# Kernel tuning notes

Hardware: AMD Instinct MI355X
Metric: run time of the kernel (lower is better)

## Reference

```python
import jax, jax.numpy as jnp
import numpy as np

HEADS = 20
HEAD_DIM = 64
NUM_IP = 20          # num_content_tokens (4) + num_style_tokens (16)
FU_SCALE = 0.5
STYLE_SCALE = 1.0
SCALE = 1.0 / np.sqrt(HEAD_DIM).astype(np.float32)


def setup_inputs() -> dict:
    key = jax.random.key(0)
    ks = jax.random.split(key, 9)
    B, S, H, C = 4, 4096, 1280, 2048
    T = 77 + NUM_IP  # text tokens + ip tokens
    w = 0.02
    return {
        "hidden_states": jax.random.normal(ks[0], (B, S, H), jnp.float32),
        "encoder_hidden_states": jax.random.normal(ks[1], (B, T, C), jnp.float32),
        "Wq": jax.random.normal(ks[2], (H, H), jnp.float32) * w,
        "Wk": jax.random.normal(ks[3], (H, C), jnp.float32) * w,
        "Wv": jax.random.normal(ks[4], (H, C), jnp.float32) * w,
        "Wk_ip": jax.random.normal(ks[5], (H, C), jnp.float32) * w,
        "Wv_ip": jax.random.normal(ks[6], (H, C), jnp.float32) * w,
        "Wo": jax.random.normal(ks[7], (H, H), jnp.float32) * w,
        "bo": jnp.zeros((H,), jnp.float32),
    }


def _to_heads(x):
    # [B, T, H] -> [B, heads, T, head_dim]
    B, T, _ = x.shape
    return x.reshape(B, T, HEADS, HEAD_DIM).transpose(0, 2, 1, 3)


def _blend(p):
    # cross-batch prob fusion: rows 1<-0, 3<-2 (CFG pairs)
    p = p.at[1].set(FU_SCALE * p[1] + (1.0 - FU_SCALE) * p[0])
    p = p.at[3].set(FU_SCALE * p[3] + (1.0 - FU_SCALE) * p[2])
    return p


def reference(hidden_states, encoder_hidden_states, Wq, Wk, Wv, Wk_ip, Wv_ip, Wo, bo):
    B, S, H = hidden_states.shape
    text = encoder_hidden_states[:, :-NUM_IP, :]   # [B, 77, C]
    ip = encoder_hidden_states[:, -NUM_IP:, :]     # [B, 20, C]

    q = _to_heads(hidden_states @ Wq.T)            # [B, h, S, d]
    k = _to_heads(text @ Wk.T)                     # [B, h, 77, d]
    v = _to_heads(text @ Wv.T)

    # fuAttn branch: explicit probs, blended across batch, then PV matmul
    probs = jax.nn.softmax(jnp.einsum('bhqd,bhkd->bhqk', q, k) * SCALE, axis=-1)
    probs = _blend(probs)
    raw = jnp.einsum('bhqk,bhkd->bhqd', probs, v)
    raw = raw.transpose(0, 2, 1, 3).reshape(B, S, H)

    # IP-adapter style cross-attention (fuIPAttn branch)
    ip_k = _to_heads(ip @ Wk_ip.T)                 # [B, h, 20, d]
    ip_v = _to_heads(ip @ Wv_ip.T)
    ip_probs = jax.nn.softmax(jnp.einsum('bhqd,bhkd->bhqk', q, ip_k) * SCALE, axis=-1)
    ip_probs = _blend(ip_probs)
    ip_hs = jnp.einsum('bhqk,bhkd->bhqd', ip_probs, ip_v)
    ip_hs = ip_hs.transpose(0, 2, 1, 3).reshape(B, S, H)

    hs = raw + STYLE_SCALE * ip_hs
    # batch rows 0 and 2 keep raw (text-only) attention output
    hs = hs.at[0].set(raw[0]).at[2].set(raw[2])

    # to_out[0] linear (bias) + to_out[1] dropout (identity at inference)
    return hs @ Wo.T + bo
```

## Files before the change

### kernel.cpp

```cpp
#include <hip/hip_runtime.h>
#include <cstdint>

typedef float floatx4 __attribute__((ext_vector_type(4)));
typedef __bf16 bf16x8 __attribute__((ext_vector_type(8)));

typedef const __attribute__((address_space(1))) void* gas_cvp;
typedef __attribute__((address_space(3))) void* las_vp;

__device__ __forceinline__ float bflo(unsigned int u) {
    return __builtin_bit_cast(float, u << 16);
}
__device__ __forceinline__ float bfhi(unsigned int u) {
    return __builtin_bit_cast(float, u & 0xffff0000u);
}
__device__ __forceinline__ unsigned short f2bf(float f) {
    unsigned int u = __builtin_bit_cast(unsigned int, f);
    u += 0x7fffu + ((u >> 16) & 1u);
    return (unsigned short)(u >> 16);
}
__device__ __forceinline__ bf16x8 ld8(const unsigned short* p) {
    return __builtin_bit_cast(bf16x8, *(const uint4*)p);
}
__device__ __forceinline__ floatx4 mfma32(bf16x8 a, bf16x8 b, floatx4 c) {
    return __builtin_amdgcn_mfma_f32_16x16x32_bf16(a, b, c, 0, 0, 0);
}
__device__ __forceinline__ void load_lds16(const void* g, void* l) {
    __builtin_amdgcn_global_load_lds(
        (gas_cvp)(unsigned long long)g,
        (las_vp)(unsigned int)(unsigned long long)l,
        16, 0, 0);
}

__global__ void cvt_f32_bf16(const float* __restrict__ in,
                             unsigned short* __restrict__ out, int n4) {
    int i = blockIdx.x * 256 + threadIdx.x;
    if (i < n4) {
        float4 v = ((const float4*)in)[i];
        ushort4 o;
        o.x = f2bf(v.x); o.y = f2bf(v.y); o.z = f2bf(v.z); o.w = f2bf(v.w);
        ((ushort4*)out)[i] = o;
    }
}

struct CvtJob { const float* src; unsigned short* dst; int n4; };
struct CvtJobs { CvtJob j[7]; };

__global__ void cvt_multi(CvtJobs jobs) {
    CvtJob jb = jobs.j[blockIdx.y];
    int i = blockIdx.x * 256 + threadIdx.x;
    if (i < jb.n4) {
        float4 v = ((const float4*)jb.src)[i];
        ushort4 o;
        o.x = f2bf(v.x); o.y = f2bf(v.y); o.z = f2bf(v.z); o.w = f2bf(v.w);
        ((ushort4*)jb.dst)[i] = o;
    }
}

struct GJob {
    const unsigned short* A;
    const unsigned short* B;
    void* C;
    int M, K;
    int rpb, bstride, roff;
    int bstart;
};
struct GArgs { GJob j[5]; };

#define GBAR() do { __builtin_amdgcn_s_barrier(); __builtin_amdgcn_sched_barrier(0); } while (0)

template <bool F32OUT>
__global__ __launch_bounds__(512, 2) void gemm256(GArgs args,
                                                  const float* __restrict__ bias) {
    const int tid = threadIdx.x;
    int jid = 0;
#pragma unroll
    for (int t = 1; t < 5; ++t)
        if ((int)blockIdx.x >= args.j[t].bstart) jid = t;
    const GJob jb = args.j[jid];
    const int K = jb.K;
    int b = (int)blockIdx.x - jb.bstart;
    {
        const int mt = (jb.M + 255) >> 8;
        const int nblk = mt * 5;
        if ((nblk & 7) == 0) b = (b & 7) * (nblk >> 3) + (b >> 3);
    }
    const int by = b / 5, bx = b - by * 5;

    __shared__ unsigned short ldsA[32768];
    __shared__ unsigned short ldsB[32768];

    const int srow   = ((tid >> 7) << 4) + ((tid >> 2) & 15);
    const int schunk = ((tid & 3) << 4) ^ (((tid >> 2) & 6) << 3);
    const int scol   = (((tid >> 6) & 1) << 5) + (schunk >> 1);

    const int Mloc = jb.M, rpbL = jb.rpb, bstrL = jb.bstride, roffL = jb.roff;
    auto maprow = [&](int r) -> size_t {
        r = (r < Mloc) ? r : (Mloc - 1);
        int blk = r / rpbL;
        return (size_t)(blk * bstrL + roffL + (r - blk * rpbL));
    };

    const unsigned short* pA[2][2];
    const unsigned short* pB[2][2];
    unsigned short* dA[2][2];
    unsigned short* dB[2][2];
#pragma unroll
    for (int h = 0; h < 2; ++h)
#pragma unroll
        for (int j = 0; j < 2; ++j) {
            const int r = h * 128 + j * 64 + srow;
            pA[h][j] = jb.A + maprow(by * 256 + r) * K + scol;
            pB[h][j] = jb.B + (size_t)(bx * 256 + r) * K + scol;
            dA[h][j] = &ldsA[h * 8192 + j * 4096 + tid * 8];
            dB[h][j] = &ldsB[h * 8192 + j * 4096 + tid * 8];
        }

    const int lane = tid & 63, fr = lane & 15, g = lane >> 4;
    const int w = tid >> 6, wr = w & 1, wc = w >> 1;
    const int rb   = fr * 32 + ((g * 8) ^ ((fr & 6) << 2));
    const int aoff = wr * 8192 + rb;
    const int boff = (wc >> 1) * 8192 + (wc & 1) * 4096 + rb;

    floatx4 acc[8][4] = {};
    bf16x8 af[4][2], bn0[2][2], bn1[2][2];

    const int KT = K >> 6;

    load_lds16(pA[0][0], dA[0][0]); load_lds16(pA[0][1], dA[0][1]);
    load_lds16(pA[1][0], dA[1][0]); load_lds16(pA[1][1], dA[1][1]);
    load_lds16(pB[0][0], dB[0][0]); load_lds16(pB[0][1], dB[0][1]);
    load_lds16(pB[1][0], dB[1][0]); load_lds16(pB[1][1], dB[1][1]);
    load_lds16(pB[0][0] + 64, dB[0][0] + 16384);
    load_lds16(pB[0][1] + 64, dB[0][1] + 16384);
    load_lds16(pA[0][0] + 64, dA[0][0] + 16384);
    load_lds16(pA[0][1] + 64, dA[0][1] + 16384);
    asm volatile("s_waitcnt vmcnt(4)" ::: "memory");
    GBAR();

    for (int u = 0; u < KT; ++u) {
        const int pb = (u & 1) << 14;
        const int qb = pb ^ 16384;
        const int k1 = (u + 1 < KT) ? (u + 1) : (KT - 1);
        const int k2 = (u + 2 < KT) ? (u + 2) : (KT - 1);

#pragma unroll
        for (int mi = 0; mi < 4; ++mi)
#pragma unroll
            for (int kk = 0; kk < 2; ++kk)
                af[mi][kk] = *(const bf16x8*)&ldsA[pb + aoff + (mi * 2 + kk) * 512];
#pragma unroll
        for (int nf = 0; nf < 2; ++nf)
#pragma unroll
            for (int kk = 0; kk < 2; ++kk)
                bn0[nf][kk] = *(const bf16x8*)&ldsB[pb + boff + (nf * 2 + kk) * 512];
        load_lds16(pA[1][0] + (size_t)k1 * 64, dA[1][0] + qb);
        load_lds16(pA[1][1] + (size_t)k1 * 64, dA[1][1] + qb);
        GBAR();
        __builtin_amdgcn_s_setprio(1);
#pragma unroll
        for (int kk = 0; kk < 2; ++kk)
#pragma unroll
            for (int mi = 0; mi < 4; ++mi)
#pragma unroll
                for (int nf = 0; nf < 2; ++nf)
                    acc[mi][nf] = mfma32(af[mi][kk], bn0[nf][kk], acc[mi][nf]);
        __builtin_amdgcn_s_setprio(0);
        GBAR();

#pragma unroll
        for (int nf = 0; nf < 2; ++nf)
#pragma unroll
            for (int kk = 0; kk < 2; ++kk)
                bn1[nf][kk] = *(const bf16x8*)&ldsB[pb + boff + ((nf + 2) * 2 + kk) * 512];
        load_lds16(pB[1][0] + (size_t)k1 * 64, dB[1][0] + qb);
        load_lds16(pB[1][1] + (size_t)k1 * 64, dB[1][1] + qb);
        GBAR();
        __builtin_amdgcn_s_setprio(1);
#pragma unroll
        for (int kk = 0; kk < 2; ++kk)
#pragma unroll
            for (int mi = 0; mi < 4; ++mi)
#pragma unroll
                for (int nf = 0; nf < 2; ++nf)
                    acc[mi][nf + 2] = mfma32(af[mi][kk], bn1[nf][kk], acc[mi][nf + 2]);
        __builtin_amdgcn_s_setprio(0);
        GBAR();

#pragma unroll
        for (int mi = 0; mi < 4; ++mi)
#pragma unroll
            for (int kk = 0; kk < 2; ++kk)
                af[mi][kk] = *(const bf16x8*)&ldsA[pb + aoff + ((mi + 4) * 2 + kk) * 512];
        load_lds16(pB[0][0] + (size_t)k2 * 64, dB[0][0] + pb);
        load_lds16(pB[0][1] + (size_t)k2 * 64, dB[0][1] + pb);
        GBAR();
        __builtin_amdgcn_s_setprio(1);
#pragma unroll
        for (int kk = 0; kk < 2; ++kk)
#pragma unroll
            for (int mi = 0; mi < 4; ++mi)
#pragma unroll
                for (int nf = 0; nf < 2; ++nf)
                    acc[mi + 4][nf + 2] = mfma32(af[mi][kk], bn1[nf][kk], acc[mi + 4][nf + 2]);
        __builtin_amdgcn_s_setprio(0);
        GBAR();

        load_lds16(pA[0][0] + (size_t)k2 * 64, dA[0][0] + pb);
        load_lds16(pA[0][1] + (size_t)k2 * 64, dA[0][1] + pb);
        GBAR();
        __builtin_amdgcn_s_setprio(1);
#pragma unroll
        for (int kk = 0; kk < 2; ++kk)
#pragma unroll
            for (int mi = 0; mi < 4; ++mi)
#pragma unroll
                for (int nf = 0; nf < 2; ++nf)
                    acc[mi + 4][nf] = mfma32(af[mi][kk], bn0[nf][kk], acc[mi + 4][nf]);
        __builtin_amdgcn_s_setprio(0);
        asm volatile("s_waitcnt vmcnt(4)" ::: "memory");
        GBAR();
    }
    asm volatile("s_waitcnt vmcnt(0)" ::: "memory");

    const int colBase = bx * 256 + wc * 64;
    const int rowBase = by * 256 + wr * 128;
    float bv[4] = {};
    if (F32OUT) {
#pragma unroll
        for (int nf = 0; nf < 4; ++nf) bv[nf] = bias[colBase + nf * 16 + fr];
    }
#pragma unroll
    for (int mi = 0; mi < 8; ++mi) {
#pragma unroll
        for (int nf = 0; nf < 4; ++nf) {
            const int col  = colBase + nf * 16 + fr;
            const int row0 = rowBase + mi * 16 + g * 4;
#pragma unroll
            for (int r = 0; r < 4; ++r) {
                const int row = row0 + r;
                if (row < Mloc) {
                    float v = acc[mi][nf][r];
                    if (F32OUT)
                        ((float*)jb.C)[(size_t)row * 1280 + col] = v + bv[nf];
                    else
                        ((unsigned short*)jb.C)[(size_t)row * 1280 + col] = f2bf(v);
                }
            }
        }
    }
}

#define NT 77
#define NI 20
#define VSTR 104
#define ISTR 40

__global__ __launch_bounds__(256, 2) void attn_mfma(
    const unsigned short* __restrict__ q,
    const unsigned short* __restrict__ kt,
    const unsigned short* __restrict__ vt,
    const unsigned short* __restrict__ kip,
    const unsigned short* __restrict__ vip,
    unsigned short* __restrict__ outp)
{
    const int tid = threadIdx.x;
    const int qt = blockIdx.x;
    const int h  = blockIdx.y;
    const int pz = blockIdx.z;
    const int b0 = 2 * pz;
    const int lane  = tid & 63;
    const int w     = tid >> 6;
    const int bi    = w >> 1;
    const int strip = (w & 1) * 16;
    const int fr = lane & 15;
    const int g  = lane >> 4;

    __shared__ unsigned short sVt[2][64][VSTR];
    __shared__ unsigned short sVipt[2][64][ISTR];
    __shared__ unsigned short sP[2][32][VSTR];

    for (int i = tid; i < 2 * 64 * (VSTR - NT); i += 256) {
        int b = i / (64 * (VSTR - NT)); int rem = i % (64 * (VSTR - NT));
        sVt[b][rem / (VSTR - NT)][NT + rem % (VSTR - NT)] = 0;
    }
    for (int i = tid; i < 2 * 64 * (ISTR - NI); i += 256) {
        int b = i / (64 * (ISTR - NI)); int rem = i % (64 * (ISTR - NI));
        sVipt[b][rem / (ISTR - NI)][NI + rem % (ISTR - NI)] = 0;
    }
    for (int i = tid; i < 2 * 32 * (VSTR - 80); i += 256) {
        int b = i / (32 * (VSTR - 80)); int rem = i % (32 * (VSTR - 80));
        sP[b][rem / (VSTR - 80)][80 + rem % (VSTR - 80)] = 0;
    }

    for (int c = tid; c < 2 * 8 * NT; c += 256) {
        int b = c / (8 * NT); int rem = c % (8 * NT);
        int dc = rem / NT; int key = rem % NT;
        uint4 v = *(const uint4*)&vt[((size_t)((b0 + b) * NT + key)) * 1280 + h * 64 + dc * 8];
        unsigned int uu[4] = {v.x, v.y, v.z, v.w};
#pragma unroll
        for (int j = 0; j < 4; j++) {
            sVt[b][dc * 8 + 2 * j][key]     = (unsigned short)(uu[j] & 0xffffu);
            sVt[b][dc * 8 + 2 * j + 1][key] = (unsigned short)(uu[j] >> 16);
        }
    }
    for (int c = tid; c < 2 * 8 * NI; c += 256) {
        int b = c / (8 * NI); int rem = c % (8 * NI);
        int dc = rem / NI; int key = rem % NI;
        uint4 v = *(const uint4*)&vip[((size_t)((b0 + b) * NI + key)) * 1280 + h * 64 + dc * 8];
        unsigned int uu[4] = {v.x, v.y, v.z, v.w};
#pragma unroll
        for (int j = 0; j < 4; j++) {
            sVipt[b][dc * 8 + 2 * j][key]     = (unsigned short)(uu[j] & 0xffffu);
            sVipt[b][dc * 8 + 2 * j + 1][key] = (unsigned short)(uu[j] >> 16);
        }
    }

    const size_t qbase = ((size_t)((b0 + bi) * 4096 + qt * 32 + strip + fr)) * 1280 + h * 64;
    bf16x8 aq0 = ld8(&q[qbase + g * 8]);
    bf16x8 aq1 = ld8(&q[qbase + 32 + g * 8]);

    floatx4 sc[5] = {};
#pragma unroll
    for (int t = 0; t < 5; t++) {
        int key = t * 16 + fr; key = (key < NT) ? key : (NT - 1);
        const size_t kb = ((size_t)((b0 + bi) * NT + key)) * 1280 + h * 64;
        sc[t] = mfma32(aq0, ld8(&kt[kb + g * 8]), sc[t]);
        sc[t] = mfma32(aq1, ld8(&kt[kb + 32 + g * 8]), sc[t]);
    }

#pragma unroll
    for (int r = 0; r < 4; r++) {
        float m = -1e30f;
#pragma unroll
        for (int t = 0; t < 5; t++) {
            float v = sc[t][r] * 0.125f;
            if (t == 4 && fr >= 13) v = -1e30f;
            sc[t][r] = v;
            m = fmaxf(m, v);
        }
        m = fmaxf(m, __shfl_xor(m, 1));
        m = fmaxf(m, __shfl_xor(m, 2));
        m = fmaxf(m, __shfl_xor(m, 4));
        m = fmaxf(m, __shfl_xor(m, 8));
        float sum = 0.f;
#pragma unroll
        for (int t = 0; t < 5; t++) {
            float e = __expf(sc[t][r] - m);
            sc[t][r] = e;
            sum += e;
        }
        sum += __shfl_xor(sum, 1);
        sum += __shfl_xor(sum, 2);
        sum += __shfl_xor(sum, 4);
        sum += __shfl_xor(sum, 8);
        float inv = 1.f / sum;
#pragma unroll
        for (int t = 0; t < 5; t++)
            sP[bi][strip + g * 4 + r][t * 16 + fr] = f2bf(sc[t][r] * inv);
    }
    __syncthreads();

    {
        unsigned int* p0 = (unsigned int*)&sP[0][0][0];
        unsigned int* p1 = (unsigned int*)&sP[1][0][0];
        for (int i = tid; i < 32 * VSTR / 2; i += 256) {
            unsigned int a = p0[i], b = p1[i];
            unsigned short r0 = f2bf(0.5f * (bflo(a) + bflo(b)));
            unsigned short r1 = f2bf(0.5f * (bfhi(a) + bfhi(b)));
            p1[i] = (unsigned int)r0 | ((unsigned int)r1 << 16);
        }
    }
    __syncthreads();

    floatx4 accO[4] = {};
    {
        const unsigned short* prow = &sP[bi][strip + fr][0];
        bf16x8 pa0 = ld8(prow + g * 8);
        bf16x8 pa1 = ld8(prow + 32 + g * 8);
        bf16x8 pa2 = ld8(prow + 64 + g * 8);
#pragma unroll
        for (int dt = 0; dt < 4; dt++) {
            const unsigned short* vrow = &sVt[bi][dt * 16 + fr][0];
            accO[dt] = mfma32(pa0, ld8(vrow + g * 8), accO[dt]);
            accO[dt] = mfma32(pa1, ld8(vrow + 32 + g * 8), accO[dt]);
            accO[dt] = mfma32(pa2, ld8(vrow + 64 + g * 8), accO[dt]);
        }
    }

    floatx4 si[2] = {};
#pragma unroll
    for (int t = 0; t < 2; t++) {
        int key = t * 16 + fr; key = (key < NI) ? key : (NI - 1);
        const size_t kb = ((size_t)((b0 + bi) * NI + key)) * 1280 + h * 64;
        si[t] = mfma32(aq0, ld8(&kip[kb + g * 8]), si[t]);
        si[t] = mfma32(aq1, ld8(&kip[kb + 32 + g * 8]), si[t]);
    }
#pragma unroll
    for (int r = 0; r < 4; r++) {
        float v0 = si[0][r] * 0.125f;
        float v1 = (fr >= 4) ? -1e30f : si[1][r] * 0.125f;
        float m = fmaxf(v0, v1);
        m = fmaxf(m, __shfl_xor(m, 1));
        m = fmaxf(m, __shfl_xor(m, 2));
        m = fmaxf(m, __shfl_xor(m, 4));
        m = fmaxf(m, __shfl_xor(m, 8));
        float e0 = __expf(v0 - m), e1 = __expf(v1 - m);
        float s = e0 + e1;
        s += __shfl_xor(s, 1);
        s += __shfl_xor(s, 2);
        s += __shfl_xor(s, 4);
        s += __shfl_xor(s, 8);
        float inv = 1.f / s;
        si[0][r] = e0 * inv;
        si[1][r] = e1 * inv;
    }
    __syncthreads();

#pragma unroll
    for (int r = 0; r < 4; r++) {
        sP[bi][strip + g * 4 + r][fr]      = f2bf(si[0][r]);
        sP[bi][strip + g * 4 + r][16 + fr] = f2bf(si[1][r]);
    }
    __syncthreads();

    for (int i = tid; i < 32 * 16; i += 256) {
        int r = i >> 4, kk = i & 15;
        unsigned int* p0 = (unsigned int*)&sP[0][r][0];
        unsigned int* p1 = (unsigned int*)&sP[1][r][0];
        unsigned int a = p0[kk], b = p1[kk];
        unsigned short r0 = f2bf(0.5f * (bflo(a) + bflo(b)));
        unsigned short r1 = f2bf(0.5f * (bfhi(a) + bfhi(b)));
        p1[kk] = (unsigned int)r0 | ((unsigned int)r1 << 16);
    }
    __syncthreads();

    if (bi == 1) {
        const unsigned short* prow = &sP[1][strip + fr][0];
        bf16x8 pip = ld8(prow + g * 8);
#pragma unroll
        for (int dt = 0; dt < 4; dt++)
            accO[dt] = mfma32(pip, ld8(&sVipt[1][dt * 16 + fr][g * 8]), accO[dt]);
    }

    const size_t orow0 = (size_t)((b0 + bi) * 4096 + qt * 32 + strip);
#pragma unroll
    for (int dt = 0; dt < 4; dt++) {
        int col = h * 64 + dt * 16 + fr;
#pragma unroll
        for (int r = 0; r < 4; r++)
            outp[(orow0 + g * 4 + r) * 1280 + col] = f2bf(accO[dt][r]);
    }
}

extern "C" void kernel_launch(void* const* d_in, const int* in_sizes, int n_in,
                              void* d_out, int out_size, void* d_ws, size_t ws_size,
                              hipStream_t stream) {
    const float* hs   = (const float*)d_in[0];
    const float* ehs  = (const float*)d_in[1];
    const float* Wq   = (const float*)d_in[2];
    const float* Wk   = (const float*)d_in[3];
    const float* Wv   = (const float*)d_in[4];
    const float* Wkip = (const float*)d_in[5];
    const float* Wvip = (const float*)d_in[6];
    const float* Wo   = (const float*)d_in[7];
    const float* bo   = (const float*)d_in[8];

    char* w = (char*)d_ws;
    size_t off = 0;
    auto alloc = [&](size_t bytes) {
        char* pp = w + off;
        off += (bytes + 255) & ~(size_t)255;
        return pp;
    };
    unsigned short* hs_bf   = (unsigned short*)alloc(16384ull * 1280 * 2);
    unsigned short* q_bf    = (unsigned short*)alloc(16384ull * 1280 * 2);
    unsigned short* at_bf   = (unsigned short*)alloc(16384ull * 1280 * 2);
    unsigned short* ehs_bf  = (unsigned short*)alloc(4ull * 97 * 2048 * 2);
    unsigned short* Wq_bf   = (unsigned short*)alloc(1280ull * 1280 * 2);
    unsigned short* Wk_bf   = (unsigned short*)alloc(1280ull * 2048 * 2);
    unsigned short* Wv_bf   = (unsigned short*)alloc(1280ull * 2048 * 2);
    unsigned short* Wkip_bf = (unsigned short*)alloc(1280ull * 2048 * 2);
    unsigned short* Wvip_bf = (unsigned short*)alloc(1280ull * 2048 * 2);
    unsigned short* Wo_bf   = (unsigned short*)alloc(1280ull * 1280 * 2);
    unsigned short* kt  = (unsigned short*)alloc(308ull * 1280 * 2);
    unsigned short* vt  = (unsigned short*)alloc(308ull * 1280 * 2);
    unsigned short* kip = (unsigned short*)alloc(80ull * 1280 * 2);
    unsigned short* vip = (unsigned short*)alloc(80ull * 1280 * 2);

    cvt_f32_bf16<<<dim3(20480, 1, 1), 256, 0, stream>>>(hs, hs_bf, 16384 * 1280 / 4);

    CvtJobs cj{};
    cj.j[0] = CvtJob{ehs,  ehs_bf,  (int)(4ull * 97 * 2048 / 4)};
    cj.j[1] = CvtJob{Wq,   Wq_bf,   1280 * 1280 / 4};
    cj.j[2] = CvtJob{Wk,   Wk_bf,   1280 * 2048 / 4};
    cj.j[3] = CvtJob{Wv,   Wv_bf,   1280 * 2048 / 4};
    cj.j[4] = CvtJob{Wkip, Wkip_bf, 1280 * 2048 / 4};
    cj.j[5] = CvtJob{Wvip, Wvip_bf, 1280 * 2048 / 4};
    cj.j[6] = CvtJob{Wo,   Wo_bf,   1280 * 1280 / 4};
    cvt_multi<<<dim3(2560, 7, 1), 256, 0, stream>>>(cj);

    GArgs g1{};
    g1.j[0] = GJob{ehs_bf, Wk_bf,   (void*)kt,    308, 2048,    77, 97,  0,  0};
    g1.j[1] = GJob{ehs_bf, Wv_bf,   (void*)vt,    308, 2048,    77, 97,  0, 10};
    g1.j[2] = GJob{ehs_bf, Wkip_bf, (void*)kip,    80, 2048,    20, 97, 77, 20};
    g1.j[3] = GJob{ehs_bf, Wvip_bf, (void*)vip,    80, 2048,    20, 97, 77, 25};
    g1.j[4] = GJob{hs_bf,  Wq_bf,   (void*)q_bf, 16384, 1280, 16384,  0,  0, 30};
    gemm256<false><<<dim3(350, 1, 1), 512, 0, stream>>>(g1, nullptr);

    attn_mfma<<<dim3(128, 20, 2), 256, 0, stream>>>(q_bf, kt, vt, kip, vip, at_bf);

    GArgs g2{};
    g2.j[0] = GJob{at_bf, Wo_bf, d_out, 16384, 1280, 16384, 0, 0, 0};
    for (int t = 1; t < 5; ++t) g2.j[t].bstart = 0x7fffffff;
    gemm256<true><<<dim3(320, 1, 1), 512, 0, stream>>>(g2, bo);
}
```

Measured before the change: 442.8 us.

## Produce transposed padded V projections in GEMM to drop LDS transpose in attention

A new conversion kernel writes zero-padded text (96 rows per batch) and IP (32 rows per batch) token buffers. The V and IP-V projections are now computed as W·Xᵀ, so the GEMM writes them already transposed. The attention kernel then reads V straight from global memory instead of building transposed copies in LDS. This removes the per-block scatter transpose and most of the shared memory, so the attention kernel now asks for 4 blocks per CU instead of 2. The cost is uncached, strided global loads of V inside the PV MFMA loop and a little extra GEMM work on the padded rows.

```diff
diff --git a/kernel.cpp b/kernel.cpp
--- a/kernel.cpp
+++ b/kernel.cpp
@@ -43,7 +43,7 @@
 }
 
 struct CvtJob { const float* src; unsigned short* dst; int n4; };
-struct CvtJobs { CvtJob j[7]; };
+struct CvtJobs { CvtJob j[6]; };
 
 __global__ void cvt_multi(CvtJobs jobs) {
     CvtJob jb = jobs.j[blockIdx.y];
@@ -56,12 +56,42 @@
     }
 }
 
+__global__ void cvt_ehs(const float* __restrict__ ehs,
+                        unsigned short* __restrict__ text,
+                        unsigned short* __restrict__ ip) {
+    int i = blockIdx.x * 256 + threadIdx.x;
+    if (i < 384 * 512) {
+        int r = i >> 9, c = i & 511;
+        int b = r / 96, t = r - b * 96;
+        ushort4 o = {0, 0, 0, 0};
+        if (t < 77) {
+            float4 v = *(const float4*)&ehs[((size_t)(b * 97 + t)) * 2048 + c * 4];
+            o.x = f2bf(v.x); o.y = f2bf(v.y); o.z = f2bf(v.z); o.w = f2bf(v.w);
+        }
+        ((ushort4*)text)[i] = o;
+    } else {
+        int i2 = i - 384 * 512;
+        if (i2 < 128 * 512) {
+            int r = i2 >> 9, c = i2 & 511;
+            int b = r >> 5, t = r & 31;
+            ushort4 o = {0, 0, 0, 0};
+            if (t < 20) {
+                float4 v = *(const float4*)&ehs[((size_t)(b * 97 + 77 + t)) * 2048 + c * 4];
+                o.x = f2bf(v.x); o.y = f2bf(v.y); o.z = f2bf(v.z); o.w = f2bf(v.w);
+            }
+            ((ushort4*)ip)[i2] = o;
+        }
+    }
+}
+
 struct GJob {
     const unsigned short* A;
     const unsigned short* B;
     void* C;
     int M, K;
-    int rpb, bstride, roff;
+    int Bn;
+    int nt;
+    int ldc;
     int bstart;
 };
 struct GArgs { GJob j[5]; };
@@ -81,10 +111,10 @@
     int b = (int)blockIdx.x - jb.bstart;
     {
         const int mt = (jb.M + 255) >> 8;
-        const int nblk = mt * 5;
+        const int nblk = mt * jb.nt;
         if ((nblk & 7) == 0) b = (b & 7) * (nblk >> 3) + (b >> 3);
     }
-    const int by = b / 5, bx = b - by * 5;
+    const int by = b / jb.nt, bx = b - by * jb.nt;
 
     __shared__ unsigned short ldsA[32768];
     __shared__ unsigned short ldsB[32768];
@@ -93,12 +123,7 @@
     const int schunk = ((tid & 3) << 4) ^ (((tid >> 2) & 6) << 3);
     const int scol   = (((tid >> 6) & 1) << 5) + (schunk >> 1);
 
-    const int Mloc = jb.M, rpbL = jb.rpb, bstrL = jb.bstride, roffL = jb.roff;
-    auto maprow = [&](int r) -> size_t {
-        r = (r < Mloc) ? r : (Mloc - 1);
-        int blk = r / rpbL;
-        return (size_t)(blk * bstrL + roffL + (r - blk * rpbL));
-    };
+    const int Mloc = jb.M, BnL = jb.Bn;
 
     const unsigned short* pA[2][2];
     const unsigned short* pB[2][2];
@@ -109,8 +134,10 @@
 #pragma unroll
         for (int j = 0; j < 2; ++j) {
             const int r = h * 128 + j * 64 + srow;
-            pA[h][j] = jb.A + maprow(by * 256 + r) * K + scol;
-            pB[h][j] = jb.B + (size_t)(bx * 256 + r) * K + scol;
+            int ra = by * 256 + r;  ra = (ra < Mloc) ? ra : (Mloc - 1);
+            int rb2 = bx * 256 + r; rb2 = (rb2 < BnL) ? rb2 : (BnL - 1);
+            pA[h][j] = jb.A + (size_t)ra * K + scol;
+            pB[h][j] = jb.B + (size_t)rb2 * K + scol;
             dA[h][j] = &ldsA[h * 8192 + j * 4096 + tid * 8];
             dB[h][j] = &ldsB[h * 8192 + j * 4096 + tid * 8];
         }
@@ -224,6 +251,7 @@
 
     const int colBase = bx * 256 + wc * 64;
     const int rowBase = by * 256 + wr * 128;
+    const int ldc = jb.ldc;
     float bv[4] = {};
     if (F32OUT) {
 #pragma unroll
@@ -241,9 +269,9 @@
                 if (row < Mloc) {
                     float v = acc[mi][nf][r];
                     if (F32OUT)
-                        ((float*)jb.C)[(size_t)row * 1280 + col] = v + bv[nf];
+                        ((float*)jb.C)[(size_t)row * ldc + col] = v + bv[nf];
                     else
-                        ((unsigned short*)jb.C)[(size_t)row * 1280 + col] = f2bf(v);
+                        ((unsigned short*)jb.C)[(size_t)row * ldc + col] = f2bf(v);
                 }
             }
         }
@@ -252,15 +280,13 @@
 
 #define NT 77
 #define NI 20
-#define VSTR 104
-#define ISTR 40
-
-__global__ __launch_bounds__(256, 2) void attn_mfma(
+
+__global__ __launch_bounds__(256, 4) void attn_mfma(
     const unsigned short* __restrict__ q,
     const unsigned short* __restrict__ kt,
-    const unsigned short* __restrict__ vt,
+    const unsigned short* __restrict__ vtT,
     const unsigned short* __restrict__ kip,
-    const unsigned short* __restrict__ vip,
+    const unsigned short* __restrict__ ipT,
     unsigned short* __restrict__ outp)
 {
     const int tid = threadIdx.x;
@@ -275,44 +301,11 @@
     const int fr = lane & 15;
     const int g  = lane >> 4;
 
-    __shared__ unsigned short sVt[2][64][VSTR];
-    __shared__ unsigned short sVipt[2][64][ISTR];
-    __shared__ unsigned short sP[2][32][VSTR];
-
-    for (int i = tid; i < 2 * 64 * (VSTR - NT); i += 256) {
-        int b = i / (64 * (VSTR - NT)); int rem = i % (64 * (VSTR - NT));
-        sVt[b][rem / (VSTR - NT)][NT + rem % (VSTR - NT)] = 0;
-    }
-    for (int i = tid; i < 2 * 64 * (ISTR - NI); i += 256) {
-        int b = i / (64 * (ISTR - NI)); int rem = i % (64 * (ISTR - NI));
-        sVipt[b][rem / (ISTR - NI)][NI + rem % (ISTR - NI)] = 0;
-    }
-    for (int i = tid; i < 2 * 32 * (VSTR - 80); i += 256) {
-        int b = i / (32 * (VSTR - 80)); int rem = i % (32 * (VSTR - 80));
-        sP[b][rem / (VSTR - 80)][80 + rem % (VSTR - 80)] = 0;
-    }
-
-    for (int c = tid; c < 2 * 8 * NT; c += 256) {
-        int b = c / (8 * NT); int rem = c % (8 * NT);
-        int dc = rem / NT; int key = rem % NT;
-        uint4 v = *(const uint4*)&vt[((size_t)((b0 + b) * NT + key)) * 1280 + h * 64 + dc * 8];
-        unsigned int uu[4] = {v.x, v.y, v.z, v.w};
-#pragma unroll
-        for (int j = 0; j < 4; j++) {
-            sVt[b][dc * 8 + 2 * j][key]     = (unsigned short)(uu[j] & 0xffffu);
-            sVt[b][dc * 8 + 2 * j + 1][key] = (unsigned short)(uu[j] >> 16);
-        }
-    }
-    for (int c = tid; c < 2 * 8 * NI; c += 256) {
-        int b = c / (8 * NI); int rem = c % (8 * NI);
-        int dc = rem / NI; int key = rem % NI;
-        uint4 v = *(const uint4*)&vip[((size_t)((b0 + b) * NI + key)) * 1280 + h * 64 + dc * 8];
-        unsigned int uu[4] = {v.x, v.y, v.z, v.w};
-#pragma unroll
-        for (int j = 0; j < 4; j++) {
-            sVipt[b][dc * 8 + 2 * j][key]     = (unsigned short)(uu[j] & 0xffffu);
-            sVipt[b][dc * 8 + 2 * j + 1][key] = (unsigned short)(uu[j] >> 16);
-        }
+    __shared__ unsigned short sP[2][32][104];
+
+    for (int i = tid; i < 2 * 32 * 24; i += 256) {
+        int b = i / (32 * 24); int rem = i % (32 * 24);
+        sP[b][rem / 24][80 + rem % 24] = 0;
     }
 
     const size_t qbase = ((size_t)((b0 + bi) * 4096 + qt * 32 + strip + fr)) * 1280 + h * 64;
@@ -322,8 +315,8 @@
     floatx4 sc[5] = {};
 #pragma unroll
     for (int t = 0; t < 5; t++) {
-        int key = t * 16 + fr; key = (key < NT) ? key : (NT - 1);
-        const size_t kb = ((size_t)((b0 + bi) * NT + key)) * 1280 + h * 64;
+        int key = t * 16 + fr;
+        const size_t kb = ((size_t)((b0 + bi) * 96 + key)) * 1280 + h * 64;
         sc[t] = mfma32(aq0, ld8(&kt[kb + g * 8]), sc[t]);
         sc[t] = mfma32(aq1, ld8(&kt[kb + 32 + g * 8]), sc[t]);
     }
@@ -363,7 +356,7 @@
     {
         unsigned int* p0 = (unsigned int*)&sP[0][0][0];
         unsigned int* p1 = (unsigned int*)&sP[1][0][0];
-        for (int i = tid; i < 32 * VSTR / 2; i += 256) {
+        for (int i = tid; i < 32 * 104 / 2; i += 256) {
             unsigned int a = p0[i], b = p1[i];
             unsigned short r0 = f2bf(0.5f * (bflo(a) + bflo(b)));
             unsigned short r1 = f2bf(0.5f * (bfhi(a) + bfhi(b)));
@@ -378,9 +371,10 @@
         bf16x8 pa0 = ld8(prow + g * 8);
         bf16x8 pa1 = ld8(prow + 32 + g * 8);
         bf16x8 pa2 = ld8(prow + 64 + g * 8);
+        const int vcol = (b0 + bi) * 96;
 #pragma unroll
         for (int dt = 0; dt < 4; dt++) {
-            const unsigned short* vrow = &sVt[bi][dt * 16 + fr][0];
+            const unsigned short* vrow = &vtT[(size_t)(h * 64 + dt * 16 + fr) * 512 + vcol];
             accO[dt] = mfma32(pa0, ld8(vrow + g * 8), accO[dt]);
             accO[dt] = mfma32(pa1, ld8(vrow + 32 + g * 8), accO[dt]);
             accO[dt] = mfma32(pa2, ld8(vrow + 64 + g * 8), accO[dt]);
@@ -390,8 +384,8 @@
     floatx4 si[2] = {};
 #pragma unroll
     for (int t = 0; t < 2; t++) {
-        int key = t * 16 + fr; key = (key < NI) ? key : (NI - 1);
-        const size_t kb = ((size_t)((b0 + bi) * NI + key)) * 1280 + h * 64;
+        int key = t * 16 + fr;
+        const size_t kb = ((size_t)((b0 + bi) * 32 + key)) * 1280 + h * 64;
         si[t] = mfma32(aq0, ld8(&kip[kb + g * 8]), si[t]);
         si[t] = mfma32(aq1, ld8(&kip[kb + 32 + g * 8]), si[t]);
     }
@@ -437,9 +431,12 @@
     if (bi == 1) {
         const unsigned short* prow = &sP[1][strip + fr][0];
         bf16x8 pip = ld8(prow + g * 8);
+        const int icol = (b0 + 1) * 32;
 #pragma unroll
         for (int dt = 0; dt < 4; dt++)
-            accO[dt] = mfma32(pip, ld8(&sVipt[1][dt * 16 + fr][g * 8]), accO[dt]);
+            accO[dt] = mfma32(pip,
+                              ld8(&ipT[(size_t)(h * 64 + dt * 16 + fr) * 256 + icol + g * 8]),
+                              accO[dt]);
     }
 
     const size_t orow0 = (size_t)((b0 + bi) * 4096 + qt * 32 + strip);
@@ -475,42 +472,44 @@
     unsigned short* hs_bf   = (unsigned short*)alloc(16384ull * 1280 * 2);
     unsigned short* q_bf    = (unsigned short*)alloc(16384ull * 1280 * 2);
     unsigned short* at_bf   = (unsigned short*)alloc(16384ull * 1280 * 2);
-    unsigned short* ehs_bf  = (unsigned short*)alloc(4ull * 97 * 2048 * 2);
+    unsigned short* text_pad= (unsigned short*)alloc(384ull * 2048 * 2);
+    unsigned short* ip_pad  = (unsigned short*)alloc(128ull * 2048 * 2);
     unsigned short* Wq_bf   = (unsigned short*)alloc(1280ull * 1280 * 2);
     unsigned short* Wk_bf   = (unsigned short*)alloc(1280ull * 2048 * 2);
     unsigned short* Wv_bf   = (unsigned short*)alloc(1280ull * 2048 * 2);
     unsigned short* Wkip_bf = (unsigned short*)alloc(1280ull * 2048 * 2);
     unsigned short* Wvip_bf = (unsigned short*)alloc(1280ull * 2048 * 2);
     unsigned short* Wo_bf   = (unsigned short*)alloc(1280ull * 1280 * 2);
-    unsigned short* kt  = (unsigned short*)alloc(308ull * 1280 * 2);
-    unsigned short* vt  = (unsigned short*)alloc(308ull * 1280 * 2);
-    unsigned short* kip = (unsigned short*)alloc(80ull * 1280 * 2);
-    unsigned short* vip = (unsigned short*)alloc(80ull * 1280 * 2);
+    unsigned short* kt  = (unsigned short*)alloc(384ull * 1280 * 2);
+    unsigned short* vtT = (unsigned short*)alloc(1280ull * 512 * 2);
+    unsigned short* kip = (unsigned short*)alloc(128ull * 1280 * 2);
+    unsigned short* ipT = (unsigned short*)alloc(1280ull * 256 * 2);
 
     cvt_f32_bf16<<<dim3(20480, 1, 1), 256, 0, stream>>>(hs, hs_bf, 16384 * 1280 / 4);
 
+    cvt_ehs<<<dim3(1024, 1, 1), 256, 0, stream>>>(ehs, text_pad, ip_pad);
+
     CvtJobs cj{};
-    cj.j[0] = CvtJob{ehs,  ehs_bf,  (int)(4ull * 97 * 2048 / 4)};
-    cj.j[1] = CvtJob{Wq,   Wq_bf,   1280 * 1280 / 4};
-    cj.j[2] = CvtJob{Wk,   Wk_bf,   1280 * 2048 / 4};
-    cj.j[3] = CvtJob{Wv,   Wv_bf,   1280 * 2048 / 4};
-    cj.j[4] = CvtJob{Wkip, Wkip_bf, 1280 * 2048 / 4};
-    cj.j[5] = CvtJob{Wvip, Wvip_bf, 1280 * 2048 / 4};
-    cj.j[6] = CvtJob{Wo,   Wo_bf,   1280 * 1280 / 4};
-    cvt_multi<<<dim3(2560, 7, 1), 256, 0, stream>>>(cj);
+    cj.j[0] = CvtJob{Wq,   Wq_bf,   1280 * 1280 / 4};
+    cj.j[1] = CvtJob{Wk,   Wk_bf,   1280 * 2048 / 4};
+    cj.j[2] = CvtJob{Wv,   Wv_bf,   1280 * 2048 / 4};
+    cj.j[3] = CvtJob{Wkip, Wkip_bf, 1280 * 2048 / 4};
+    cj.j[4] = CvtJob{Wvip, Wvip_bf, 1280 * 2048 / 4};
+    cj.j[5] = CvtJob{Wo,   Wo_bf,   1280 * 1280 / 4};
+    cvt_multi<<<dim3(2560, 6, 1), 256, 0, stream>>>(cj);
 
     GArgs g1{};
-    g1.j[0] = GJob{ehs_bf, Wk_bf,   (void*)kt,    308, 2048,    77, 97,  0,  0};
-    g1.j[1] = GJob{ehs_bf, Wv_bf,   (void*)vt,    308, 2048,    77, 97,  0, 10};
-    g1.j[2] = GJob{ehs_bf, Wkip_bf, (void*)kip,    80, 2048,    20, 97, 77, 20};
-    g1.j[3] = GJob{ehs_bf, Wvip_bf, (void*)vip,    80, 2048,    20, 97, 77, 25};
-    g1.j[4] = GJob{hs_bf,  Wq_bf,   (void*)q_bf, 16384, 1280, 16384,  0,  0, 30};
+    g1.j[0] = GJob{text_pad, Wk_bf,   (void*)kt,    384, 2048, 1280, 5, 1280,  0};
+    g1.j[1] = GJob{ip_pad,   Wkip_bf, (void*)kip,   128, 2048, 1280, 5, 1280, 10};
+    g1.j[2] = GJob{Wv_bf,    text_pad,(void*)vtT,  1280, 2048,  384, 2,  512, 15};
+    g1.j[3] = GJob{Wvip_bf,  ip_pad,  (void*)ipT,  1280, 2048,  128, 1,  256, 25};
+    g1.j[4] = GJob{hs_bf,    Wq_bf,   (void*)q_bf,16384, 1280, 1280, 5, 1280, 30};
     gemm256<false><<<dim3(350, 1, 1), 512, 0, stream>>>(g1, nullptr);
 
-    attn_mfma<<<dim3(128, 20, 2), 256, 0, stream>>>(q_bf, kt, vt, kip, vip, at_bf);
+    attn_mfma<<<dim3(128, 20, 2), 256, 0, stream>>>(q_bf, kt, vtT, kip, ipT, at_bf);
 
     GArgs g2{};
-    g2.j[0] = GJob{at_bf, Wo_bf, d_out, 16384, 1280, 16384, 0, 0, 0};
+    g2.j[0] = GJob{at_bf, Wo_bf, d_out, 16384, 1280, 1280, 5, 1280, 0};
     for (int t = 1; t < 5; ++t) g2.j[t].bstart = 0x7fffffff;
     gemm256<true><<<dim3(320, 1, 1), 512, 0, stream>>>(g2, bo);
 }
```

After: 440.1 us. About the same (-0.6%).
